# Kernel tuning notes

Measured on AMD Instinct MI355X. Metric: run time of the kernel, lower is better.

The kernel has to match this reference:

```python
import jax, jax.numpy as jnp
import numpy as np

B, S, D, H, W = 2, 8192, 512, 8, 256   # batch, seq, d_model, heads, one-sided window
HD = D // H                            # head dim = 64
C = S // W                             # number of chunks of size W (seq % 2W == 0 holds)


def setup_inputs() -> dict:
    key = jax.random.key(0)
    ks = jax.random.split(key, 7)
    x = jax.random.normal(ks[0], (B, S, D), jnp.float32)
    def w(k):
        return jax.random.normal(k, (D, D), jnp.float32) * 0.02
    def b(k):
        return jax.random.normal(k, (D,), jnp.float32) * 0.02
    return {
        "x": x,
        "Wq": w(ks[1]), "bq": b(ks[2]),
        "Wk": w(ks[3]), "bk": b(ks[4]),
        "Wv": w(ks[5]), "bv": b(ks[6]),
    }


def _heads_chunked(t):
    # (B,S,D) -> (B*H, C, W, HD): split heads, then split sequence into chunks of W
    return t.reshape(B, S, H, HD).transpose(0, 2, 1, 3).reshape(B * H, C, W, HD)


def _three_chunks(t):
    # neighbor-chunk concat: for chunk c, gather chunks [c-1, c, c+1] (zero padded at ends)
    tp = jnp.pad(t, ((0, 0), (1, 1), (0, 0), (0, 0)))
    return jnp.concatenate([tp[:, :-2], tp[:, 1:-1], tp[:, 2:]], axis=2)  # (B*H, C, 3W, HD)


def reference(x, Wq, bq, Wk, bk, Wv, bv):
    scale = 1.0 / np.sqrt(HD)
    q = _heads_chunked((x @ Wq + bq) * scale)
    k = _heads_chunked(x @ Wk + bk)
    v = _heads_chunked(x @ Wv + bv)

    k3 = _three_chunks(k)
    v3 = _three_chunks(v)

    # chunk-local scores against 3 neighboring chunks: (B*H, C, W, 3W)
    scores = jnp.einsum('bcxd,bcyd->bcxy', q, k3)

    # extract the (2W+1)-wide diagonal band: query x attends keys x..x+2W in the 3W window
    rows = jnp.arange(W)[:, None]                       # (W,1)
    diag = rows + jnp.arange(2 * W + 1)[None, :]        # (W, 2W+1) indices into 3W axis
    band = jnp.take_along_axis(scores, diag[None, None], axis=3)  # (B*H, C, W, 2W+1)

    # mask band entries whose global key position falls outside [0, S)
    pos = jnp.arange(S).reshape(C, W)[:, :, None] + (jnp.arange(2 * W + 1) - W)  # (C,W,2W+1)
    valid = (pos >= 0) & (pos < S)
    band = jnp.where(valid[None], band, -jnp.inf)

    probs = jax.nn.softmax(band, axis=-1)  # (B*H, C, W, 2W+1)

    # scatter band probs back into (W, 3W) layout and contract with values
    full = jnp.zeros((B * H, C, W, 3 * W), probs.dtype).at[:, :, rows, diag].set(probs)
    out = jnp.einsum('bcxy,bcyd->bcxd', full, v3)  # (B*H, C, W, HD)

    return out.reshape(B, H, S, HD).transpose(0, 2, 1, 3).reshape(B, S, D)
```

## Files before the change

### kernel.cpp

```cpp
#include <hip/hip_runtime.h>
#include <hip/hip_bf16.h>

#define S_LEN 8192
#define D_MODEL 512
#define NH 8
#define HD 64
#define WIN 256
#define NB 2

typedef __hip_bfloat16 bf16;
typedef __attribute__((ext_vector_type(8))) short short8;
typedef __attribute__((ext_vector_type(4))) float f32x4;

static __device__ __forceinline__ short f2bf(float f) {
    bf16 h = __float2bfloat16(f);
    return *reinterpret_cast<short*>(&h);
}

static __device__ __forceinline__ void gload_lds16(short* lds, const short* g) {
    __builtin_amdgcn_global_load_lds(
        (const __attribute__((address_space(1))) void*)g,
        (__attribute__((address_space(3))) void*)lds, 16, 0, 0);
}

__global__ __launch_bounds__(256) void convert_x_kernel(
    const float* __restrict__ x, short* __restrict__ xb)
{
    const int n4 = (NB * S_LEN * D_MODEL) / 4;
    for (int i = blockIdx.x * 256 + threadIdx.x; i < n4; i += gridDim.x * 256) {
        float4 v = ((const float4*)x)[i];
        short4 o;
        o.x = f2bf(v.x); o.y = f2bf(v.y); o.z = f2bf(v.z); o.w = f2bf(v.w);
        ((short4*)xb)[i] = o;
    }
}

__global__ __launch_bounds__(256) void convert_wT_kernel(
    const float* __restrict__ Wq, const float* __restrict__ Wk,
    const float* __restrict__ Wv, short* __restrict__ wT)
{
    __shared__ float t[32][33];
    const float* W = blockIdx.z == 0 ? Wq : (blockIdx.z == 1 ? Wk : Wv);
    const int n0 = blockIdx.x * 32, k0 = blockIdx.y * 32;
    const int tx = threadIdx.x & 31, ty = threadIdx.x >> 5;
#pragma unroll
    for (int i = 0; i < 4; ++i)
        t[ty + 8 * i][tx] = W[(size_t)(k0 + ty + 8 * i) * D_MODEL + n0 + tx];
    __syncthreads();
#pragma unroll
    for (int i = 0; i < 4; ++i) {
        const int nl = ty + 8 * i, kl = tx;
        wT[(size_t)blockIdx.z * D_MODEL * D_MODEL +
           (size_t)(n0 + nl) * D_MODEL + k0 + kl] = f2bf(t[kl][nl]);
    }
}

__global__ __launch_bounds__(256) void proj_mfma_kernel(
    const short* __restrict__ xb, const short* __restrict__ wT,
    const float* __restrict__ bq, const float* __restrict__ bk,
    const float* __restrict__ bv, bf16* __restrict__ qkv)
{
    __shared__ short Ash[128 * 64];
    __shared__ short Bsh[128 * 64];

    const int widx = blockIdx.x >> 2;
    const int col0 = (blockIdx.x & 3) * 128;
    const int row0 = blockIdx.y * 128;
    const int tid  = threadIdx.x;
    const int w    = tid >> 6;
    const int lane = tid & 63;
    const int col  = lane & 15;
    const int kg   = lane >> 4;

    const float* bias = widx == 0 ? bq : (widx == 1 ? bk : bv);
    const float scale = widx == 0 ? 0.125f : 1.0f;
    const short* wbase = wT + (size_t)widx * D_MODEL * D_MODEL;

    const f32x4 zero4 = {0.f, 0.f, 0.f, 0.f};
    f32x4 acc[4][4];
#pragma unroll
    for (int i = 0; i < 4; ++i)
#pragma unroll
        for (int j = 0; j < 4; ++j) acc[i][j] = zero4;

    const int wm0 = (w >> 1) * 64;
    const int wn0 = (w & 1) * 64;

    for (int kb = 0; kb < D_MODEL; kb += 64) {
#pragma unroll
        for (int ci = 0; ci < 4; ++ci) {
            const int Lb = w * 256 + ci * 64;
            const int L  = Lb + lane;
            const int m  = L >> 3;
            const int kc = ((L & 7) - (m >> 1)) & 7;
            const int ko = kb + kc * 8;
            gload_lds16(Ash + (size_t)Lb * 8,
                        xb + (size_t)(row0 + m) * D_MODEL + ko);
            gload_lds16(Bsh + (size_t)Lb * 8,
                        wbase + (size_t)(col0 + m) * D_MODEL + ko);
        }
        __syncthreads();

#pragma unroll
        for (int s = 0; s < 2; ++s) {
            short8 af[4], bfr[4];
#pragma unroll
            for (int mt = 0; mt < 4; ++mt) {
                const int m = wm0 + mt * 16 + col;
                const int c = m * 8 + ((s * 4 + kg + (m >> 1)) & 7);
                af[mt] = *(const short8*)(Ash + (size_t)c * 8);
            }
#pragma unroll
            for (int nt = 0; nt < 4; ++nt) {
                const int n = wn0 + nt * 16 + col;
                const int c = n * 8 + ((s * 4 + kg + (n >> 1)) & 7);
                bfr[nt] = *(const short8*)(Bsh + (size_t)c * 8);
            }
#pragma unroll
            for (int mt = 0; mt < 4; ++mt)
#pragma unroll
                for (int nt = 0; nt < 4; ++nt)
                    acc[mt][nt] = __builtin_amdgcn_mfma_f32_16x16x32_bf16(
                        af[mt], bfr[nt], acc[mt][nt], 0, 0, 0);
        }
        __syncthreads();
    }

    bf16* dst = qkv + (size_t)widx * (NB * NH * S_LEN * HD);
#pragma unroll
    for (int nt = 0; nt < 4; ++nt) {
        const int n = col0 + wn0 + nt * 16 + col;
        const float bias_v = bias[n];
        const int h = n >> 6, d = n & 63;
#pragma unroll
        for (int mt = 0; mt < 4; ++mt) {
            const int m0 = row0 + wm0 + mt * 16 + kg * 4;
            const int b = m0 >> 13, s0 = m0 & (S_LEN - 1);
            if (widx == 2) {
                short4 pk;
                pk.x = f2bf(acc[mt][nt][0] + bias_v);
                pk.y = f2bf(acc[mt][nt][1] + bias_v);
                pk.z = f2bf(acc[mt][nt][2] + bias_v);
                pk.w = f2bf(acc[mt][nt][3] + bias_v);
                *(short4*)&dst[(((size_t)(b * NH + h)) * HD + d) * S_LEN + s0] = pk;
            } else {
#pragma unroll
                for (int r = 0; r < 4; ++r)
                    dst[(((size_t)(b * NH + h)) * S_LEN + s0 + r) * HD + d] =
                        __float2bfloat16((acc[mt][nt][r] + bias_v) * scale);
            }
        }
    }
}

__global__ __launch_bounds__(256) void proj_kernel(
    const float* __restrict__ x, const float* __restrict__ Wm,
    const float* __restrict__ bias, bf16* __restrict__ dst, float scale,
    int transpose_v)
{
    __shared__ float As[16][64];
    __shared__ float Bs[16][64];
    const int tid  = threadIdx.x;
    const int row0 = blockIdx.y * 64;
    const int col0 = blockIdx.x * 64;
    const int ty = tid >> 4, tx = tid & 15;
    const int t4 = tid * 4;
    const int ai = t4 >> 4, aj = t4 & 15;
    const int bj = t4 >> 6, bi = t4 & 63;
    float acc[4][4] = {};
    for (int kb = 0; kb < D_MODEL; kb += 16) {
        float4 av = *(const float4*)(x  + (size_t)(row0 + ai) * D_MODEL + kb + aj);
        float4 bv = *(const float4*)(Wm + (size_t)(kb + bj)  * D_MODEL + col0 + bi);
        As[aj + 0][ai] = av.x; As[aj + 1][ai] = av.y;
        As[aj + 2][ai] = av.z; As[aj + 3][ai] = av.w;
        *(float4*)(&Bs[bj][bi]) = bv;
        __syncthreads();
#pragma unroll
        for (int k = 0; k < 16; ++k) {
            float a[4], b[4];
#pragma unroll
            for (int ii = 0; ii < 4; ++ii) a[ii] = As[k][ty * 4 + ii];
#pragma unroll
            for (int jj = 0; jj < 4; ++jj) b[jj] = Bs[k][tx * 4 + jj];
#pragma unroll
            for (int ii = 0; ii < 4; ++ii)
#pragma unroll
                for (int jj = 0; jj < 4; ++jj) acc[ii][jj] += a[ii] * b[jj];
        }
        __syncthreads();
    }
#pragma unroll
    for (int ii = 0; ii < 4; ++ii) {
        const int m = row0 + ty * 4 + ii;
        const int b = m >> 13, s = m & (S_LEN - 1);
#pragma unroll
        for (int jj = 0; jj < 4; ++jj) {
            const int n = col0 + tx * 4 + jj;
            const int h = n >> 6, d = n & 63;
            const float v = (acc[ii][jj] + bias[n]) * scale;
            if (transpose_v)
                dst[(((size_t)(b * NH + h)) * HD + d) * S_LEN + s] = __float2bfloat16(v);
            else
                dst[(((size_t)(b * NH + h)) * S_LEN + s) * HD + d] = __float2bfloat16(v);
        }
    }
}

__global__ __launch_bounds__(256) void attn_mfma3_kernel(
    const bf16* __restrict__ qw, const bf16* __restrict__ kw,
    const bf16* __restrict__ vt, float* __restrict__ out)
{
    __shared__ __align__(16) short Ksh[2][4096];
    __shared__ __align__(16) short Vsh[2][4096];
    __shared__ __align__(16) short Psh[4][16][72];

    const int bh   = blockIdx.x;
    const int qt0  = blockIdx.y * 64;
    const int tid  = threadIdx.x;
    const int w    = tid >> 6;
    const int lane = tid & 63;
    const int col  = lane & 15;
    const int kg   = lane >> 4;
    const int q0   = qt0 + w * 16;
    const int q    = q0 + col;
    const size_t base = (size_t)bh * S_LEN * HD;

    const short* qg  = (const short*)qw;
    const short* kgp = (const short*)kw;
    const short* vgp = (const short*)vt;

    const int kt_lo = qt0 - WIN < 0 ? 0 : qt0 - WIN;
    const int kt_hi = qt0 + WIN > S_LEN - 64 ? S_LEN - 64 : qt0 + WIN;
    const int NT    = ((kt_hi - kt_lo) >> 6) + 1;

    const int p0   = tid;
    const int p1   = tid + 256;
    const int r0   = p0 >> 3, c0 = (p0 & 7) ^ (r0 & 7);
    const int r1   = p1 >> 3, c1 = (p1 & 7) ^ (r1 & 7);
    const int ldsb0 = w * 64 * 8;
    const int ldsb1 = (w * 64 + 256) * 8;

    const short* qptr = qg + base + (size_t)q * HD + kg * 8;
    const short8 qB0 = *(const short8*)(qptr);
    const short8 qB1 = *(const short8*)(qptr + 32);

    const f32x4 zero4 = {0.f, 0.f, 0.f, 0.f};
    f32x4 Oacc[4] = {zero4, zero4, zero4, zero4};
    float m = -1e30f, l = 0.f;

    const int x7 = col & 7;

    {
        const int kt = kt_lo;
        gload_lds16(&Ksh[0][ldsb0], kgp + base + (size_t)(kt + r0) * HD + c0 * 8);
        gload_lds16(&Ksh[0][ldsb1], kgp + base + (size_t)(kt + r1) * HD + c1 * 8);
        gload_lds16(&Vsh[0][ldsb0], vgp + base + (size_t)r0 * S_LEN + kt + c0 * 8);
        gload_lds16(&Vsh[0][ldsb1], vgp + base + (size_t)r1 * S_LEN + kt + c1 * 8);
    }

    for (int i = 0; i < NT; ++i) {
        __syncthreads();

        if (i + 1 < NT) {
            const int kt = kt_lo + 64 * (i + 1);
            const int nb = (i + 1) & 1;
            gload_lds16(&Ksh[nb][ldsb0], kgp + base + (size_t)(kt + r0) * HD + c0 * 8);
            gload_lds16(&Ksh[nb][ldsb1], kgp + base + (size_t)(kt + r1) * HD + c1 * 8);
            gload_lds16(&Vsh[nb][ldsb0], vgp + base + (size_t)r0 * S_LEN + kt + c0 * 8);
            gload_lds16(&Vsh[nb][ldsb1], vgp + base + (size_t)r1 * S_LEN + kt + c1 * 8);
        }

        const int kt = kt_lo + 64 * i;
        const short* Kb = Ksh[i & 1];
        const short* Vb = Vsh[i & 1];

        f32x4 sc[4];
#pragma unroll
        for (int t = 0; t < 4; ++t) {
            const int key = 16 * t + col;
            const short8 kA0 = *(const short8*)(Kb + (size_t)(key * 8 + (kg ^ x7)) * 8);
            const short8 kA1 = *(const short8*)(Kb + (size_t)(key * 8 + ((kg + 4) ^ x7)) * 8);
            f32x4 a = zero4;
            a = __builtin_amdgcn_mfma_f32_16x16x32_bf16(kA0, qB0, a, 0, 0, 0);
            a = __builtin_amdgcn_mfma_f32_16x16x32_bf16(kA1, qB1, a, 0, 0, 0);
            sc[t] = a;
        }

        const bool need_mask = (kt == qt0 - WIN) || (kt == qt0 + WIN);
        if (need_mask) {
#pragma unroll
            for (int t = 0; t < 4; ++t)
#pragma unroll
                for (int r = 0; r < 4; ++r) {
                    const int j = kt + 16 * t + kg * 4 + r;
                    if (j < q - WIN || j > q + WIN) sc[t][r] = -1e30f;
                }
        }

        float tmax = -1e30f;
#pragma unroll
        for (int t = 0; t < 4; ++t)
#pragma unroll
            for (int r = 0; r < 4; ++r) tmax = fmaxf(tmax, sc[t][r]);
        tmax = fmaxf(tmax, __shfl_xor(tmax, 16));
        tmax = fmaxf(tmax, __shfl_xor(tmax, 32));
        const float mnew = fmaxf(m, tmax);
        const float alpha = __expf(m - mnew);
        m = mnew;

        float p[4][4];
        float rs = 0.f;
        if (need_mask) {
#pragma unroll
            for (int t = 0; t < 4; ++t)
#pragma unroll
                for (int r = 0; r < 4; ++r) {
                    const float pv = (sc[t][r] > -1e29f) ? __expf(sc[t][r] - mnew) : 0.f;
                    p[t][r] = pv; rs += pv;
                }
        } else {
#pragma unroll
            for (int t = 0; t < 4; ++t)
#pragma unroll
                for (int r = 0; r < 4; ++r) {
                    const float pv = __expf(sc[t][r] - mnew);
                    p[t][r] = pv; rs += pv;
                }
        }
        rs += __shfl_xor(rs, 16);
        rs += __shfl_xor(rs, 32);
        l = l * alpha + rs;

#pragma unroll
        for (int t = 0; t < 4; ++t) {
            short4 pk;
            pk.x = f2bf(p[t][0]); pk.y = f2bf(p[t][1]);
            pk.z = f2bf(p[t][2]); pk.w = f2bf(p[t][3]);
            *(short4*)&Psh[w][col][16 * t + 4 * kg] = pk;
        }

#pragma unroll
        for (int dt = 0; dt < 4; ++dt)
#pragma unroll
            for (int r = 0; r < 4; ++r) Oacc[dt][r] *= alpha;

        const short* pp = &Psh[w][col][kg * 8];
        const short8 pB0 = *(const short8*)(pp);
        const short8 pB1 = *(const short8*)(pp + 32);

#pragma unroll
        for (int dt = 0; dt < 4; ++dt) {
            const int d = dt * 16 + col;
            const short8 vA0 = *(const short8*)(Vb + (size_t)(d * 8 + (kg ^ x7)) * 8);
            const short8 vA1 = *(const short8*)(Vb + (size_t)(d * 8 + ((kg + 4) ^ x7)) * 8);
            Oacc[dt] = __builtin_amdgcn_mfma_f32_16x16x32_bf16(vA0, pB0, Oacc[dt], 0, 0, 0);
            Oacc[dt] = __builtin_amdgcn_mfma_f32_16x16x32_bf16(vA1, pB1, Oacc[dt], 0, 0, 0);
        }
    }

    const float inv = 1.0f / l;
    const int b = bh >> 3, h = bh & 7;
    float* op = out + ((size_t)(b * S_LEN + q)) * D_MODEL + h * HD + kg * 4;
#pragma unroll
    for (int dt = 0; dt < 4; ++dt) {
        float4 o;
        o.x = Oacc[dt][0] * inv; o.y = Oacc[dt][1] * inv;
        o.z = Oacc[dt][2] * inv; o.w = Oacc[dt][3] * inv;
        *(float4*)(op + dt * 16) = o;
    }
}

extern "C" void kernel_launch(void* const* d_in, const int* in_sizes, int n_in,
                              void* d_out, int out_size, void* d_ws, size_t ws_size,
                              hipStream_t stream)
{
    const float* x  = (const float*)d_in[0];
    const float* Wq = (const float*)d_in[1];
    const float* bq = (const float*)d_in[2];
    const float* Wk = (const float*)d_in[3];
    const float* bk = (const float*)d_in[4];
    const float* Wv = (const float*)d_in[5];
    const float* bv = (const float*)d_in[6];
    float* out = (float*)d_out;

    const size_t n_elem = (size_t)NB * NH * S_LEN * HD;
    bf16* qw = (bf16*)d_ws;
    bf16* kw = qw + n_elem;
    bf16* vw = kw + n_elem;
    short* xb = (short*)(vw + n_elem);
    short* wT = xb + (size_t)NB * S_LEN * D_MODEL;

    const size_t need = (3 * n_elem + (size_t)NB * S_LEN * D_MODEL +
                         3 * (size_t)D_MODEL * D_MODEL) * sizeof(short);

    if (ws_size >= need) {
        convert_x_kernel<<<2048, 256, 0, stream>>>(x, xb);
        dim3 wgrid(D_MODEL / 32, D_MODEL / 32, 3);
        convert_wT_kernel<<<wgrid, 256, 0, stream>>>(Wq, Wk, Wv, wT);
        dim3 ggrid(12, (NB * S_LEN) / 128);
        proj_mfma_kernel<<<ggrid, 256, 0, stream>>>(xb, wT, bq, bk, bv, qw);
    } else {
        dim3 pgrid(D_MODEL / 64, (NB * S_LEN) / 64);
        proj_kernel<<<pgrid, 256, 0, stream>>>(x, Wq, bq, qw, 0.125f, 0);
        proj_kernel<<<pgrid, 256, 0, stream>>>(x, Wk, bk, kw, 1.0f, 0);
        proj_kernel<<<pgrid, 256, 0, stream>>>(x, Wv, bv, vw, 1.0f, 1);
    }

    dim3 agrid(NB * NH, S_LEN / 64);
    attn_mfma3_kernel<<<agrid, 256, 0, stream>>>(qw, kw, vw, out);
}
```

Baseline: 183.3 us.

## Load V fragments directly from global into registers and swap grid axes

The V tile no longer passes through LDS. Each wave loads its V MFMA operands from the transposed V buffer in global memory straight into registers at the start of each key tile, while K keeps its double-buffered LDS staging. The launch grid axes are also swapped so that consecutive blocks walk along the sequence within one head, which should improve L2 reuse of the overlapping K/V windows. The trade-off is that V loads are issued inside the loop with no prefetch, so their latency may be exposed, and every wave now reloads the same V data from cache instead of sharing it through LDS.

```diff
diff --git a/kernel.cpp b/kernel.cpp
--- a/kernel.cpp
+++ b/kernel.cpp
@@ -206,16 +206,15 @@
     }
 }
 
-__global__ __launch_bounds__(256) void attn_mfma3_kernel(
+__global__ __launch_bounds__(256) void attn_mfma4_kernel(
     const bf16* __restrict__ qw, const bf16* __restrict__ kw,
     const bf16* __restrict__ vt, float* __restrict__ out)
 {
     __shared__ __align__(16) short Ksh[2][4096];
-    __shared__ __align__(16) short Vsh[2][4096];
     __shared__ __align__(16) short Psh[4][16][72];
 
-    const int bh   = blockIdx.x;
-    const int qt0  = blockIdx.y * 64;
+    const int bh   = blockIdx.y;
+    const int qt0  = blockIdx.x * 64;
     const int tid  = threadIdx.x;
     const int w    = tid >> 6;
     const int lane = tid & 63;
@@ -233,10 +232,9 @@
     const int kt_hi = qt0 + WIN > S_LEN - 64 ? S_LEN - 64 : qt0 + WIN;
     const int NT    = ((kt_hi - kt_lo) >> 6) + 1;
 
-    const int p0   = tid;
-    const int p1   = tid + 256;
-    const int r0   = p0 >> 3, c0 = (p0 & 7) ^ (r0 & 7);
-    const int r1   = p1 >> 3, c1 = (p1 & 7) ^ (r1 & 7);
+    const int p0 = tid, p1 = tid + 256;
+    const int r0 = p0 >> 3, c0 = (p0 & 7) ^ (r0 & 7);
+    const int r1 = p1 >> 3, c1 = (p1 & 7) ^ (r1 & 7);
     const int ldsb0 = w * 64 * 8;
     const int ldsb1 = (w * 64 + 256) * 8;
 
@@ -250,29 +248,30 @@
 
     const int x7 = col & 7;
 
-    {
-        const int kt = kt_lo;
-        gload_lds16(&Ksh[0][ldsb0], kgp + base + (size_t)(kt + r0) * HD + c0 * 8);
-        gload_lds16(&Ksh[0][ldsb1], kgp + base + (size_t)(kt + r1) * HD + c1 * 8);
-        gload_lds16(&Vsh[0][ldsb0], vgp + base + (size_t)r0 * S_LEN + kt + c0 * 8);
-        gload_lds16(&Vsh[0][ldsb1], vgp + base + (size_t)r1 * S_LEN + kt + c1 * 8);
-    }
+    gload_lds16(&Ksh[0][ldsb0], kgp + base + (size_t)(kt_lo + r0) * HD + c0 * 8);
+    gload_lds16(&Ksh[0][ldsb1], kgp + base + (size_t)(kt_lo + r1) * HD + c1 * 8);
 
     for (int i = 0; i < NT; ++i) {
         __syncthreads();
 
+        const int kt = kt_lo + 64 * i;
+
+        short8 vA0[4], vA1[4];
+#pragma unroll
+        for (int dt = 0; dt < 4; ++dt) {
+            const short* vp = vgp + base + (size_t)(dt * 16 + col) * S_LEN + kt + kg * 8;
+            vA0[dt] = *(const short8*)(vp);
+            vA1[dt] = *(const short8*)(vp + 32);
+        }
+
         if (i + 1 < NT) {
-            const int kt = kt_lo + 64 * (i + 1);
+            const int ktn = kt_lo + 64 * (i + 1);
             const int nb = (i + 1) & 1;
-            gload_lds16(&Ksh[nb][ldsb0], kgp + base + (size_t)(kt + r0) * HD + c0 * 8);
-            gload_lds16(&Ksh[nb][ldsb1], kgp + base + (size_t)(kt + r1) * HD + c1 * 8);
-            gload_lds16(&Vsh[nb][ldsb0], vgp + base + (size_t)r0 * S_LEN + kt + c0 * 8);
-            gload_lds16(&Vsh[nb][ldsb1], vgp + base + (size_t)r1 * S_LEN + kt + c1 * 8);
-        }
-
-        const int kt = kt_lo + 64 * i;
+            gload_lds16(&Ksh[nb][ldsb0], kgp + base + (size_t)(ktn + r0) * HD + c0 * 8);
+            gload_lds16(&Ksh[nb][ldsb1], kgp + base + (size_t)(ktn + r1) * HD + c1 * 8);
+        }
+
         const short* Kb = Ksh[i & 1];
-        const short* Vb = Vsh[i & 1];
 
         f32x4 sc[4];
 #pragma unroll
@@ -350,11 +349,8 @@
 
 #pragma unroll
         for (int dt = 0; dt < 4; ++dt) {
-            const int d = dt * 16 + col;
-            const short8 vA0 = *(const short8*)(Vb + (size_t)(d * 8 + (kg ^ x7)) * 8);
-            const short8 vA1 = *(const short8*)(Vb + (size_t)(d * 8 + ((kg + 4) ^ x7)) * 8);
-            Oacc[dt] = __builtin_amdgcn_mfma_f32_16x16x32_bf16(vA0, pB0, Oacc[dt], 0, 0, 0);
-            Oacc[dt] = __builtin_amdgcn_mfma_f32_16x16x32_bf16(vA1, pB1, Oacc[dt], 0, 0, 0);
+            Oacc[dt] = __builtin_amdgcn_mfma_f32_16x16x32_bf16(vA0[dt], pB0, Oacc[dt], 0, 0, 0);
+            Oacc[dt] = __builtin_amdgcn_mfma_f32_16x16x32_bf16(vA1[dt], pB1, Oacc[dt], 0, 0, 0);
         }
     }
 
@@ -406,6 +402,6 @@
         proj_kernel<<<pgrid, 256, 0, stream>>>(x, Wv, bv, vw, 1.0f, 1);
     }
 
-    dim3 agrid(NB * NH, S_LEN / 64);
-    attn_mfma3_kernel<<<agrid, 256, 0, stream>>>(qw, kw, vw, out);
-}
+    dim3 agrid(S_LEN / 64, NB * NH);
+    attn_mfma4_kernel<<<agrid, 256, 0, stream>>>(qw, kw, vw, out);
+}
```

Result: slower. 219.2 us (+19.5%).

## Enlarge attention query tile to 128 rows with 512-thread blocks

Applied to the files above, without the earlier changes.

The attention kernel now handles 128 queries per block with 8 waves instead of 64 queries with 4 waves, so each K/V tile staged in LDS is shared by twice as many queries. Each thread issues one async global-to-LDS load per tensor per tile instead of two. The key range grows by one tile, which adds some masked work at the edges, and the masking test is now computed per wave. The intent is to cut K/V global traffic and loop overhead per query, at the cost of larger blocks and more partially masked tiles.

```diff
diff --git a/kernel.cpp b/kernel.cpp
--- a/kernel.cpp
+++ b/kernel.cpp
@@ -206,16 +206,16 @@
     }
 }
 
-__global__ __launch_bounds__(256) void attn_mfma3_kernel(
+__global__ __launch_bounds__(512) void attn_mfma5_kernel(
     const bf16* __restrict__ qw, const bf16* __restrict__ kw,
     const bf16* __restrict__ vt, float* __restrict__ out)
 {
     __shared__ __align__(16) short Ksh[2][4096];
     __shared__ __align__(16) short Vsh[2][4096];
-    __shared__ __align__(16) short Psh[4][16][72];
+    __shared__ __align__(16) short Psh[8][16][72];
 
     const int bh   = blockIdx.x;
-    const int qt0  = blockIdx.y * 64;
+    const int qt0  = blockIdx.y * 128;
     const int tid  = threadIdx.x;
     const int w    = tid >> 6;
     const int lane = tid & 63;
@@ -230,15 +230,12 @@
     const short* vgp = (const short*)vt;
 
     const int kt_lo = qt0 - WIN < 0 ? 0 : qt0 - WIN;
-    const int kt_hi = qt0 + WIN > S_LEN - 64 ? S_LEN - 64 : qt0 + WIN;
+    const int kt_hi0 = qt0 + WIN + 64;
+    const int kt_hi = kt_hi0 > S_LEN - 64 ? S_LEN - 64 : kt_hi0;
     const int NT    = ((kt_hi - kt_lo) >> 6) + 1;
 
-    const int p0   = tid;
-    const int p1   = tid + 256;
-    const int r0   = p0 >> 3, c0 = (p0 & 7) ^ (r0 & 7);
-    const int r1   = p1 >> 3, c1 = (p1 & 7) ^ (r1 & 7);
-    const int ldsb0 = w * 64 * 8;
-    const int ldsb1 = (w * 64 + 256) * 8;
+    const int r0 = tid >> 3, c0 = (tid & 7) ^ (r0 & 7);
+    const int ldsb = w * 64 * 8;
 
     const short* qptr = qg + base + (size_t)q * HD + kg * 8;
     const short8 qB0 = *(const short8*)(qptr);
@@ -250,24 +247,17 @@
 
     const int x7 = col & 7;
 
-    {
-        const int kt = kt_lo;
-        gload_lds16(&Ksh[0][ldsb0], kgp + base + (size_t)(kt + r0) * HD + c0 * 8);
-        gload_lds16(&Ksh[0][ldsb1], kgp + base + (size_t)(kt + r1) * HD + c1 * 8);
-        gload_lds16(&Vsh[0][ldsb0], vgp + base + (size_t)r0 * S_LEN + kt + c0 * 8);
-        gload_lds16(&Vsh[0][ldsb1], vgp + base + (size_t)r1 * S_LEN + kt + c1 * 8);
-    }
+    gload_lds16(&Ksh[0][ldsb], kgp + base + (size_t)(kt_lo + r0) * HD + c0 * 8);
+    gload_lds16(&Vsh[0][ldsb], vgp + base + (size_t)r0 * S_LEN + kt_lo + c0 * 8);
 
     for (int i = 0; i < NT; ++i) {
         __syncthreads();
 
         if (i + 1 < NT) {
-            const int kt = kt_lo + 64 * (i + 1);
+            const int ktn = kt_lo + 64 * (i + 1);
             const int nb = (i + 1) & 1;
-            gload_lds16(&Ksh[nb][ldsb0], kgp + base + (size_t)(kt + r0) * HD + c0 * 8);
-            gload_lds16(&Ksh[nb][ldsb1], kgp + base + (size_t)(kt + r1) * HD + c1 * 8);
-            gload_lds16(&Vsh[nb][ldsb0], vgp + base + (size_t)r0 * S_LEN + kt + c0 * 8);
-            gload_lds16(&Vsh[nb][ldsb1], vgp + base + (size_t)r1 * S_LEN + kt + c1 * 8);
+            gload_lds16(&Ksh[nb][ldsb], kgp + base + (size_t)(ktn + r0) * HD + c0 * 8);
+            gload_lds16(&Vsh[nb][ldsb], vgp + base + (size_t)r0 * S_LEN + ktn + c0 * 8);
         }
 
         const int kt = kt_lo + 64 * i;
@@ -286,7 +276,7 @@
             sc[t] = a;
         }
 
-        const bool need_mask = (kt == qt0 - WIN) || (kt == qt0 + WIN);
+        const bool need_mask = (kt < q0 + 15 - WIN) || (kt + 63 > q0 + WIN);
         if (need_mask) {
 #pragma unroll
             for (int t = 0; t < 4; ++t)
@@ -406,6 +396,6 @@
         proj_kernel<<<pgrid, 256, 0, stream>>>(x, Wv, bv, vw, 1.0f, 1);
     }
 
-    dim3 agrid(NB * NH, S_LEN / 64);
-    attn_mfma3_kernel<<<agrid, 256, 0, stream>>>(qw, kw, vw, out);
-}
+    dim3 agrid(NB * NH, S_LEN / 128);
+    attn_mfma5_kernel<<<agrid, 512, 0, stream>>>(qw, kw, vw, out);
+}
```

Result: no change. 180.6 us (-1.5%).
